# Performance work log

Measured on AMD Instinct MI355X. Metric: run time of the kernel, lower is better.

Reference implementation:

```python
import jax, jax.numpy as jnp
import numpy as np

RANK = 16
ALPHA = 16.0
IN_F = 4096
OUT_F = 11008
TOKENS = 64


def setup_inputs() -> dict:
    key = jax.random.key(0)
    k_x, k_w, k_s, k_a, k_b, k_bias = jax.random.split(key, 6)
    return {
        "x": jax.random.normal(k_x, (TOKENS, IN_F), dtype=jnp.float32),
        "weight_int4": jax.random.normal(k_w, (OUT_F, IN_F), dtype=jnp.float32),
        "weight_scale": jax.random.uniform(k_s, (OUT_F,), dtype=jnp.float32),
        "lora_A": jax.random.normal(k_a, (RANK, IN_F), dtype=jnp.float32) * 0.01,
        "lora_B": jax.random.normal(k_b, (OUT_F, RANK), dtype=jnp.float32),
        "bias": jax.random.normal(k_bias, (OUT_F,), dtype=jnp.float32),
    }


def reference(x, weight_int4, weight_scale, lora_A, lora_B, bias):
    # Dequantize: per-output-channel scale.  [out, in]
    weight = weight_int4 * weight_scale[:, None]
    # LoRA delta: B @ A scaled by alpha/rank.  [out, in]
    lora_weight = (lora_B @ lora_A) * (ALPHA / RANK)
    effective_weight = weight + lora_weight
    # F.linear: x @ W^T + b  ->  [tokens, out]
    return x @ effective_weight.T + bias
```

## Files before the change

### kernel.cpp

```cpp
#include <hip/hip_runtime.h>
#include <hip/hip_bf16.h>
#include <cstdint>

#define TOK   64
#define INF   4096
#define OUTF  11008
#define NBLK  172
#define SPLITK 4
#define KCHUNKS 128
#define KCPQ  32

using bf16x8  = __attribute__((ext_vector_type(8))) __bf16;
using floatx4 = __attribute__((ext_vector_type(4))) float;

union B8u { uint32_t u[4]; uint4 q; bf16x8 v; };

__device__ __forceinline__ uint32_t hi2(float a, float b) {
    return (__float_as_uint(a) >> 16) | (__float_as_uint(b) & 0xffff0000u);
}
__device__ __forceinline__ float losub(float x) {
    return x - __uint_as_float(__float_as_uint(x) & 0xffff0000u);
}

__global__ __launch_bounds__(256) void k_prep_x(const float* __restrict__ x,
        unsigned short* __restrict__ xh, unsigned short* __restrict__ xl) {
    int idx  = blockIdx.x * 256 + threadIdx.x;
    int j    = idx & 7;
    int lane = (idx >> 3) & 63;
    int kc   = (idx >> 9) & 127;
    int mt   = idx >> 16;
    int row  = mt * 16 + (lane & 15);
    int col  = kc * 32 + ((lane >> 4) << 3) + j;
    float v  = x[(size_t)row * INF + col];
    uint32_t u = __float_as_uint(v);
    float lo = losub(v);
    xh[idx] = (unsigned short)(u >> 16);
    xl[idx] = (unsigned short)(__float_as_uint(lo) >> 16);
}

__global__ __launch_bounds__(64) void k_lora_t(const float* __restrict__ x,
        const float* __restrict__ A, float* __restrict__ tm) {
    int t = blockIdx.x >> 4, r = blockIdx.x & 15, lane = threadIdx.x;
    const float4* xr = (const float4*)(x + (size_t)t * INF);
    const float4* ar = (const float4*)(A + (size_t)r * INF);
    float s = 0.f;
    for (int i = lane; i < INF / 4; i += 64) {
        float4 a = xr[i], b = ar[i];
        s += a.x * b.x + a.y * b.y + a.z * b.z + a.w * b.w;
    }
#pragma unroll
    for (int off = 32; off > 0; off >>= 1) s += __shfl_down(s, off);
    if (lane == 0) tm[t * 16 + r] = s;
}

template<bool ATOMIC>
__global__ __launch_bounds__(256) void k_main(const float* __restrict__ W,
        const uint4* __restrict__ xh, const uint4* __restrict__ xl,
        const float* __restrict__ scale, float* __restrict__ part,
        float* __restrict__ out) {
    int lane = threadIdx.x & 63;
    int wv   = threadIdx.x >> 6;
    int nb   = blockIdx.x % NBLK;
    int q    = blockIdx.x / NBLK;
    int orow = nb * 64 + wv * 16 + (lane & 15);
    int quad = lane >> 4;

    const float* wp = W + (size_t)orow * INF + q * (KCPQ * 32) + quad * 8;

    floatx4 acc[4] = {};

#pragma unroll 2
    for (int kc = 0; kc < KCPQ; ++kc) {
        float4 w0 = *(const float4*)(wp + (size_t)kc * 32);
        float4 w1 = *(const float4*)(wp + (size_t)kc * 32 + 4);
        B8u wh, wl;
        wh.u[0] = hi2(w0.x, w0.y);  wh.u[1] = hi2(w0.z, w0.w);
        wh.u[2] = hi2(w1.x, w1.y);  wh.u[3] = hi2(w1.z, w1.w);
        wl.u[0] = hi2(losub(w0.x), losub(w0.y));
        wl.u[1] = hi2(losub(w0.z), losub(w0.w));
        wl.u[2] = hi2(losub(w1.x), losub(w1.y));
        wl.u[3] = hi2(losub(w1.z), losub(w1.w));

        int base = (q * KCPQ + kc) * 64 + lane;
#pragma unroll
        for (int mt = 0; mt < 4; ++mt) {
            B8u ah, al;
            ah.q = xh[mt * 8192 + base];
            al.q = xl[mt * 8192 + base];
            acc[mt] = __builtin_amdgcn_mfma_f32_16x16x32_bf16(ah.v, wh.v, acc[mt], 0, 0, 0);
            acc[mt] = __builtin_amdgcn_mfma_f32_16x16x32_bf16(ah.v, wl.v, acc[mt], 0, 0, 0);
            acc[mt] = __builtin_amdgcn_mfma_f32_16x16x32_bf16(al.v, wh.v, acc[mt], 0, 0, 0);
        }
    }

#pragma unroll
    for (int mt = 0; mt < 4; ++mt) {
        int token = mt * 16 + quad * 4;
#pragma unroll
        for (int r = 0; r < 4; ++r) {
            if constexpr (ATOMIC) {
                float sc = scale[orow];
                atomicAdd(&out[(size_t)(token + r) * OUTF + orow], sc * acc[mt][r]);
            } else {
                part[((size_t)q * TOK + token + r) * OUTF + orow] = acc[mt][r];
            }
        }
    }
}

__global__ __launch_bounds__(256) void k_post(const float* __restrict__ part,
        const float* __restrict__ scale, const float* __restrict__ bias,
        const float* __restrict__ lB, const float* __restrict__ tm,
        float* __restrict__ out) {
    int o = blockIdx.x * 256 + threadIdx.x;
    int t = blockIdx.y;
    if (o >= OUTF) return;
    float s = 0.f;
#pragma unroll
    for (int qq = 0; qq < SPLITK; ++qq)
        s += part[((size_t)qq * TOK + t) * OUTF + o];
    const float4* Br = (const float4*)(lB + (size_t)o * 16);
    const float4* tr = (const float4*)(tm + (size_t)t * 16);
    float l = 0.f;
#pragma unroll
    for (int i = 0; i < 4; ++i) {
        float4 b = Br[i], tt = tr[i];
        l += b.x * tt.x + b.y * tt.y + b.z * tt.z + b.w * tt.w;
    }
    out[(size_t)t * OUTF + o] = s * scale[o] + l + bias[o];
}

__global__ __launch_bounds__(256) void k_pre(const float* __restrict__ bias,
        const float* __restrict__ lB, const float* __restrict__ tm,
        float* __restrict__ out) {
    int o = blockIdx.x * 256 + threadIdx.x;
    int t = blockIdx.y;
    if (o >= OUTF) return;
    const float4* Br = (const float4*)(lB + (size_t)o * 16);
    const float4* tr = (const float4*)(tm + (size_t)t * 16);
    float l = 0.f;
#pragma unroll
    for (int i = 0; i < 4; ++i) {
        float4 b = Br[i], tt = tr[i];
        l += b.x * tt.x + b.y * tt.y + b.z * tt.z + b.w * tt.w;
    }
    out[(size_t)t * OUTF + o] = l + bias[o];
}

extern "C" void kernel_launch(void* const* d_in, const int* in_sizes, int n_in,
                              void* d_out, int out_size, void* d_ws, size_t ws_size,
                              hipStream_t stream) {
    const float* x     = (const float*)d_in[0];
    const float* W     = (const float*)d_in[1];
    const float* scale = (const float*)d_in[2];
    const float* lA    = (const float*)d_in[3];
    const float* lB    = (const float*)d_in[4];
    const float* bias  = (const float*)d_in[5];
    float* out = (float*)d_out;

    char* ws = (char*)d_ws;
    unsigned short* xh = (unsigned short*)(ws);
    unsigned short* xl = (unsigned short*)(ws + 524288);
    float* tm   = (float*)(ws + 1048576);
    float* part = (float*)(ws + 1052672);
    const size_t need = 1052672 + (size_t)SPLITK * TOK * OUTF * 4;

    k_prep_x<<<1024, 256, 0, stream>>>(x, xh, xl);
    k_lora_t<<<1024, 64, 0, stream>>>(x, lA, tm);

    if (ws_size >= need) {
        k_main<false><<<NBLK * SPLITK, 256, 0, stream>>>(W, (const uint4*)xh,
                (const uint4*)xl, scale, part, out);
        k_post<<<dim3(43, TOK), 256, 0, stream>>>(part, scale, bias, lB, tm, out);
    } else {
        k_pre<<<dim3(43, TOK), 256, 0, stream>>>(bias, lB, tm, out);
        k_main<true><<<NBLK * SPLITK, 256, 0, stream>>>(W, (const uint4*)xh,
                (const uint4*)xl, scale, nullptr, out);
    }
}
```

Before: 328.8 us.

## Prefetch weight chunks in registers, raise split-K to 8, share x in LoRA kernel

The main GEMM kernel now keeps a four-deep register ring of fp32 weight loads, issuing the next chunk's loads before converting and multiplying the current one, so memory latency overlaps with MFMA work. Split-K rises from 4 to 8 when workspace allows, doubling the block count to 1376 to better fill the CUs for this memory-bound weight stream. The cost is twice the partial-sum traffic in the reduction kernel. The LoRA projection kernel stages each token's x row in shared memory and computes all 16 ranks per block, cutting redundant x reads.

```diff
diff --git a/kernel.cpp b/kernel.cpp
--- a/kernel.cpp
+++ b/kernel.cpp
@@ -6,9 +6,7 @@
 #define INF   4096
 #define OUTF  11008
 #define NBLK  172
-#define SPLITK 4
 #define KCHUNKS 128
-#define KCPQ  32
 
 using bf16x8  = __attribute__((ext_vector_type(8))) __bf16;
 using floatx4 = __attribute__((ext_vector_type(4))) float;
@@ -38,26 +36,35 @@
     xl[idx] = (unsigned short)(__float_as_uint(lo) >> 16);
 }
 
-__global__ __launch_bounds__(64) void k_lora_t(const float* __restrict__ x,
+__global__ __launch_bounds__(256) void k_lora_t(const float* __restrict__ x,
         const float* __restrict__ A, float* __restrict__ tm) {
-    int t = blockIdx.x >> 4, r = blockIdx.x & 15, lane = threadIdx.x;
+    __shared__ float4 xs[INF / 4];
+    int t = blockIdx.x, tid = threadIdx.x;
     const float4* xr = (const float4*)(x + (size_t)t * INF);
-    const float4* ar = (const float4*)(A + (size_t)r * INF);
-    float s = 0.f;
-    for (int i = lane; i < INF / 4; i += 64) {
-        float4 a = xr[i], b = ar[i];
-        s += a.x * b.x + a.y * b.y + a.z * b.z + a.w * b.w;
-    }
-#pragma unroll
-    for (int off = 32; off > 0; off >>= 1) s += __shfl_down(s, off);
-    if (lane == 0) tm[t * 16 + r] = s;
-}
-
-template<bool ATOMIC>
+    for (int i = tid; i < INF / 4; i += 256) xs[i] = xr[i];
+    __syncthreads();
+    int wv = tid >> 6, lane = tid & 63;
+#pragma unroll
+    for (int rr = 0; rr < 4; ++rr) {
+        int r = wv * 4 + rr;
+        const float4* ar = (const float4*)(A + (size_t)r * INF);
+        float s = 0.f;
+        for (int i = lane; i < INF / 4; i += 64) {
+            float4 a = xs[i], b = ar[i];
+            s += a.x * b.x + a.y * b.y + a.z * b.z + a.w * b.w;
+        }
+#pragma unroll
+        for (int off = 32; off > 0; off >>= 1) s += __shfl_down(s, off);
+        if (lane == 0) tm[t * 16 + r] = s;
+    }
+}
+
+template<int QCNT, bool ATOMIC>
 __global__ __launch_bounds__(256) void k_main(const float* __restrict__ W,
         const uint4* __restrict__ xh, const uint4* __restrict__ xl,
         const float* __restrict__ scale, float* __restrict__ part,
         float* __restrict__ out) {
+    constexpr int KC = KCHUNKS / QCNT;
     int lane = threadIdx.x & 63;
     int wv   = threadIdx.x >> 6;
     int nb   = blockIdx.x % NBLK;
@@ -65,31 +72,49 @@
     int orow = nb * 64 + wv * 16 + (lane & 15);
     int quad = lane >> 4;
 
-    const float* wp = W + (size_t)orow * INF + q * (KCPQ * 32) + quad * 8;
+    const float* wp = W + (size_t)orow * INF + q * (KC * 32) + quad * 8;
+    int xoff = q * KC * 64 + lane;
 
     floatx4 acc[4] = {};
 
-#pragma unroll 2
-    for (int kc = 0; kc < KCPQ; ++kc) {
-        float4 w0 = *(const float4*)(wp + (size_t)kc * 32);
-        float4 w1 = *(const float4*)(wp + (size_t)kc * 32 + 4);
-        B8u wh, wl;
-        wh.u[0] = hi2(w0.x, w0.y);  wh.u[1] = hi2(w0.z, w0.w);
-        wh.u[2] = hi2(w1.x, w1.y);  wh.u[3] = hi2(w1.z, w1.w);
-        wl.u[0] = hi2(losub(w0.x), losub(w0.y));
-        wl.u[1] = hi2(losub(w0.z), losub(w0.w));
-        wl.u[2] = hi2(losub(w1.x), losub(w1.y));
-        wl.u[3] = hi2(losub(w1.z), losub(w1.w));
-
-        int base = (q * KCPQ + kc) * 64 + lane;
-#pragma unroll
-        for (int mt = 0; mt < 4; ++mt) {
-            B8u ah, al;
-            ah.q = xh[mt * 8192 + base];
-            al.q = xl[mt * 8192 + base];
-            acc[mt] = __builtin_amdgcn_mfma_f32_16x16x32_bf16(ah.v, wh.v, acc[mt], 0, 0, 0);
-            acc[mt] = __builtin_amdgcn_mfma_f32_16x16x32_bf16(ah.v, wl.v, acc[mt], 0, 0, 0);
-            acc[mt] = __builtin_amdgcn_mfma_f32_16x16x32_bf16(al.v, wh.v, acc[mt], 0, 0, 0);
+    constexpr int D = 4;
+    float4 wA[D], wB[D];
+#pragma unroll
+    for (int d = 0; d < D; ++d) {
+        wA[d] = *(const float4*)(wp + d * 32);
+        wB[d] = *(const float4*)(wp + d * 32 + 4);
+    }
+
+#pragma unroll 1
+    for (int base = 0; base < KC; base += D) {
+#pragma unroll
+        for (int d = 0; d < D; ++d) {
+            int kc = base + d;
+            int xbase = xoff + kc * 64;
+            B8u ah[4], al[4];
+#pragma unroll
+            for (int mt = 0; mt < 4; ++mt) {
+                ah[mt].q = xh[mt * 8192 + xbase];
+                al[mt].q = xl[mt * 8192 + xbase];
+            }
+            float4 w0 = wA[d], w1 = wB[d];
+            if (base + D < KC) {
+                wA[d] = *(const float4*)(wp + (size_t)(base + D + d) * 32);
+                wB[d] = *(const float4*)(wp + (size_t)(base + D + d) * 32 + 4);
+            }
+            B8u wh, wl;
+            wh.u[0] = hi2(w0.x, w0.y);  wh.u[1] = hi2(w0.z, w0.w);
+            wh.u[2] = hi2(w1.x, w1.y);  wh.u[3] = hi2(w1.z, w1.w);
+            wl.u[0] = hi2(losub(w0.x), losub(w0.y));
+            wl.u[1] = hi2(losub(w0.z), losub(w0.w));
+            wl.u[2] = hi2(losub(w1.x), losub(w1.y));
+            wl.u[3] = hi2(losub(w1.z), losub(w1.w));
+#pragma unroll
+            for (int mt = 0; mt < 4; ++mt) {
+                acc[mt] = __builtin_amdgcn_mfma_f32_16x16x32_bf16(ah[mt].v, wh.v, acc[mt], 0, 0, 0);
+                acc[mt] = __builtin_amdgcn_mfma_f32_16x16x32_bf16(ah[mt].v, wl.v, acc[mt], 0, 0, 0);
+                acc[mt] = __builtin_amdgcn_mfma_f32_16x16x32_bf16(al[mt].v, wh.v, acc[mt], 0, 0, 0);
+            }
         }
     }
 
@@ -99,8 +124,7 @@
 #pragma unroll
         for (int r = 0; r < 4; ++r) {
             if constexpr (ATOMIC) {
-                float sc = scale[orow];
-                atomicAdd(&out[(size_t)(token + r) * OUTF + orow], sc * acc[mt][r]);
+                atomicAdd(&out[(size_t)(token + r) * OUTF + orow], scale[orow] * acc[mt][r]);
             } else {
                 part[((size_t)q * TOK + token + r) * OUTF + orow] = acc[mt][r];
             }
@@ -108,6 +132,7 @@
     }
 }
 
+template<int QCNT>
 __global__ __launch_bounds__(256) void k_post(const float* __restrict__ part,
         const float* __restrict__ scale, const float* __restrict__ bias,
         const float* __restrict__ lB, const float* __restrict__ tm,
@@ -117,7 +142,7 @@
     if (o >= OUTF) return;
     float s = 0.f;
 #pragma unroll
-    for (int qq = 0; qq < SPLITK; ++qq)
+    for (int qq = 0; qq < QCNT; ++qq)
         s += part[((size_t)qq * TOK + t) * OUTF + o];
     const float4* Br = (const float4*)(lB + (size_t)o * 16);
     const float4* tr = (const float4*)(tm + (size_t)t * 16);
@@ -163,18 +188,24 @@
     unsigned short* xl = (unsigned short*)(ws + 524288);
     float* tm   = (float*)(ws + 1048576);
     float* part = (float*)(ws + 1052672);
-    const size_t need = 1052672 + (size_t)SPLITK * TOK * OUTF * 4;
+    const size_t base_ws = 1052672;
+    const size_t need8 = base_ws + 8ull * TOK * OUTF * 4;
+    const size_t need4 = base_ws + 4ull * TOK * OUTF * 4;
 
     k_prep_x<<<1024, 256, 0, stream>>>(x, xh, xl);
-    k_lora_t<<<1024, 64, 0, stream>>>(x, lA, tm);
-
-    if (ws_size >= need) {
-        k_main<false><<<NBLK * SPLITK, 256, 0, stream>>>(W, (const uint4*)xh,
+    k_lora_t<<<TOK, 256, 0, stream>>>(x, lA, tm);
+
+    if (ws_size >= need8) {
+        k_main<8, false><<<NBLK * 8, 256, 0, stream>>>(W, (const uint4*)xh,
                 (const uint4*)xl, scale, part, out);
-        k_post<<<dim3(43, TOK), 256, 0, stream>>>(part, scale, bias, lB, tm, out);
+        k_post<8><<<dim3(43, TOK), 256, 0, stream>>>(part, scale, bias, lB, tm, out);
+    } else if (ws_size >= need4) {
+        k_main<4, false><<<NBLK * 4, 256, 0, stream>>>(W, (const uint4*)xh,
+                (const uint4*)xl, scale, part, out);
+        k_post<4><<<dim3(43, TOK), 256, 0, stream>>>(part, scale, bias, lB, tm, out);
     } else {
         k_pre<<<dim3(43, TOK), 256, 0, stream>>>(bias, lB, tm, out);
-        k_main<true><<<NBLK * SPLITK, 256, 0, stream>>>(W, (const uint4*)xh,
+        k_main<8, true><<<NBLK * 8, 256, 0, stream>>>(W, (const uint4*)xh,
                 (const uint4*)xl, scale, nullptr, out);
     }
 }
```

Result: no change. 334.7 us (+1.8%).

## Stage x tiles in LDS, widen split-K to 16, two output tiles per wave

Applied to the files above, without the earlier changes.

The main GEMM kernel now splits K 16 ways with 8 k-chunks per block. The x hi/lo bf16 tiles are loaded once into shared memory via global_load_lds, and all W loads for the chunk are issued up front. Each wave computes two 16-row output tiles, so x fragments are reused across more rows. The LoRA projection kernel is reorganised into 256-thread blocks with a fully unrolled loop. In exchange, partial-sum traffic grows (16 partial buffers of 64x11008 floats read by the post kernel), and more registers are needed to hold the prefetched W.

```diff
diff --git a/kernel.cpp b/kernel.cpp
--- a/kernel.cpp
+++ b/kernel.cpp
@@ -5,10 +5,10 @@
 #define TOK   64
 #define INF   4096
 #define OUTF  11008
-#define NBLK  172
-#define SPLITK 4
 #define KCHUNKS 128
-#define KCPQ  32
+#define QCNT  16
+#define KC    8
+#define NBLK2 86
 
 using bf16x8  = __attribute__((ext_vector_type(8))) __bf16;
 using floatx4 = __attribute__((ext_vector_type(4))) float;
@@ -20,6 +20,14 @@
 }
 __device__ __forceinline__ float losub(float x) {
     return x - __uint_as_float(__float_as_uint(x) & 0xffff0000u);
+}
+__device__ __forceinline__ void packW(float4 a, float4 b, B8u& wh, B8u& wl) {
+    wh.u[0] = hi2(a.x, a.y);  wh.u[1] = hi2(a.z, a.w);
+    wh.u[2] = hi2(b.x, b.y);  wh.u[3] = hi2(b.z, b.w);
+    wl.u[0] = hi2(losub(a.x), losub(a.y));
+    wl.u[1] = hi2(losub(a.z), losub(a.w));
+    wl.u[2] = hi2(losub(b.x), losub(b.y));
+    wl.u[3] = hi2(losub(b.z), losub(b.w));
 }
 
 __global__ __launch_bounds__(256) void k_prep_x(const float* __restrict__ x,
@@ -38,14 +46,16 @@
     xl[idx] = (unsigned short)(__float_as_uint(lo) >> 16);
 }
 
-__global__ __launch_bounds__(64) void k_lora_t(const float* __restrict__ x,
+__global__ __launch_bounds__(256) void k_lora_t(const float* __restrict__ x,
         const float* __restrict__ A, float* __restrict__ tm) {
-    int t = blockIdx.x >> 4, r = blockIdx.x & 15, lane = threadIdx.x;
+    int t = blockIdx.x, wv = threadIdx.x >> 6, lane = threadIdx.x & 63;
+    int r = blockIdx.y * 4 + wv;
     const float4* xr = (const float4*)(x + (size_t)t * INF);
     const float4* ar = (const float4*)(A + (size_t)r * INF);
     float s = 0.f;
-    for (int i = lane; i < INF / 4; i += 64) {
-        float4 a = xr[i], b = ar[i];
+#pragma unroll
+    for (int i = 0; i < INF / 4 / 64; ++i) {
+        float4 a = xr[lane + i * 64], b = ar[lane + i * 64];
         s += a.x * b.x + a.y * b.y + a.z * b.z + a.w * b.w;
     }
 #pragma unroll
@@ -54,42 +64,62 @@
 }
 
 template<bool ATOMIC>
-__global__ __launch_bounds__(256) void k_main(const float* __restrict__ W,
+__global__ __launch_bounds__(256, 2) void k_main(const float* __restrict__ W,
         const uint4* __restrict__ xh, const uint4* __restrict__ xl,
         const float* __restrict__ scale, float* __restrict__ part,
         float* __restrict__ out) {
-    int lane = threadIdx.x & 63;
-    int wv   = threadIdx.x >> 6;
-    int nb   = blockIdx.x % NBLK;
-    int q    = blockIdx.x / NBLK;
-    int orow = nb * 64 + wv * 16 + (lane & 15);
+    __shared__ uint4 xs[2][4][KC][64];
+
+    int tid  = threadIdx.x;
+    int lane = tid & 63;
+    int wv   = tid >> 6;
+    int nb   = blockIdx.x % NBLK2;
+    int q    = blockIdx.x / NBLK2;
     int quad = lane >> 4;
-
-    const float* wp = W + (size_t)orow * INF + q * (KCPQ * 32) + quad * 8;
-
-    floatx4 acc[4] = {};
-
-#pragma unroll 2
-    for (int kc = 0; kc < KCPQ; ++kc) {
-        float4 w0 = *(const float4*)(wp + (size_t)kc * 32);
-        float4 w1 = *(const float4*)(wp + (size_t)kc * 32 + 4);
-        B8u wh, wl;
-        wh.u[0] = hi2(w0.x, w0.y);  wh.u[1] = hi2(w0.z, w0.w);
-        wh.u[2] = hi2(w1.x, w1.y);  wh.u[3] = hi2(w1.z, w1.w);
-        wl.u[0] = hi2(losub(w0.x), losub(w0.y));
-        wl.u[1] = hi2(losub(w0.z), losub(w0.w));
-        wl.u[2] = hi2(losub(w1.x), losub(w1.y));
-        wl.u[3] = hi2(losub(w1.z), losub(w1.w));
-
-        int base = (q * KCPQ + kc) * 64 + lane;
+    int ch0  = nb * 128 + wv * 32 + (lane & 15);
+
+#pragma unroll
+    for (int i = 0; i < 16; ++i) {
+        int c  = wv * 16 + i;
+        int hl = c >> 5, mt = (c >> 3) & 3, kc = c & 7;
+        const uint4* g = (hl ? xl : xh)
+                       + ((size_t)mt * KCHUNKS + q * KC + kc) * 64 + lane;
+        __builtin_amdgcn_global_load_lds(
+            (const __attribute__((address_space(1))) uint32_t*)g,
+            (__attribute__((address_space(3))) uint32_t*)&xs[hl][mt][kc][0],
+            16, 0, 0);
+    }
+    __syncthreads();
+
+    const float* wp0 = W + (size_t)ch0 * INF + q * (KC * 32) + quad * 8;
+    const float* wp1 = wp0 + (size_t)16 * INF;
+    float4 w0a[KC], w0b[KC], w1a[KC], w1b[KC];
+#pragma unroll
+    for (int kc = 0; kc < KC; ++kc) {
+        w0a[kc] = *(const float4*)(wp0 + kc * 32);
+        w0b[kc] = *(const float4*)(wp0 + kc * 32 + 4);
+        w1a[kc] = *(const float4*)(wp1 + kc * 32);
+        w1b[kc] = *(const float4*)(wp1 + kc * 32 + 4);
+    }
+
+    floatx4 acc0[4] = {}, acc1[4] = {};
+
+#pragma unroll
+    for (int kc = 0; kc < KC; ++kc) {
+        B8u wh0, wl0, wh1, wl1;
+        packW(w0a[kc], w0b[kc], wh0, wl0);
+        packW(w1a[kc], w1b[kc], wh1, wl1);
 #pragma unroll
         for (int mt = 0; mt < 4; ++mt) {
             B8u ah, al;
-            ah.q = xh[mt * 8192 + base];
-            al.q = xl[mt * 8192 + base];
-            acc[mt] = __builtin_amdgcn_mfma_f32_16x16x32_bf16(ah.v, wh.v, acc[mt], 0, 0, 0);
-            acc[mt] = __builtin_amdgcn_mfma_f32_16x16x32_bf16(ah.v, wl.v, acc[mt], 0, 0, 0);
-            acc[mt] = __builtin_amdgcn_mfma_f32_16x16x32_bf16(al.v, wh.v, acc[mt], 0, 0, 0);
+            ah.q = xs[0][mt][kc][lane];
+            al.q = xs[1][mt][kc][lane];
+            acc0[mt] = __builtin_amdgcn_mfma_f32_16x16x32_bf16(ah.v, wh0.v, acc0[mt], 0, 0, 0);
+            acc0[mt] = __builtin_amdgcn_mfma_f32_16x16x32_bf16(ah.v, wl0.v, acc0[mt], 0, 0, 0);
+            acc0[mt] = __builtin_amdgcn_mfma_f32_16x16x32_bf16(al.v, wh0.v, acc0[mt], 0, 0, 0);
+            acc1[mt] = __builtin_amdgcn_mfma_f32_16x16x32_bf16(ah.v, wh1.v, acc1[mt], 0, 0, 0);
+            acc1[mt] = __builtin_amdgcn_mfma_f32_16x16x32_bf16(ah.v, wl1.v, acc1[mt], 0, 0, 0);
+            acc1[mt] = __builtin_amdgcn_mfma_f32_16x16x32_bf16(al.v, wh1.v, acc1[mt], 0, 0, 0);
         }
     }
 
@@ -99,10 +129,11 @@
 #pragma unroll
         for (int r = 0; r < 4; ++r) {
             if constexpr (ATOMIC) {
-                float sc = scale[orow];
-                atomicAdd(&out[(size_t)(token + r) * OUTF + orow], sc * acc[mt][r]);
+                atomicAdd(&out[(size_t)(token + r) * OUTF + ch0], scale[ch0] * acc0[mt][r]);
+                atomicAdd(&out[(size_t)(token + r) * OUTF + ch0 + 16], scale[ch0 + 16] * acc1[mt][r]);
             } else {
-                part[((size_t)q * TOK + token + r) * OUTF + orow] = acc[mt][r];
+                part[((size_t)q * TOK + token + r) * OUTF + ch0]      = acc0[mt][r];
+                part[((size_t)q * TOK + token + r) * OUTF + ch0 + 16] = acc1[mt][r];
             }
         }
     }
@@ -117,7 +148,7 @@
     if (o >= OUTF) return;
     float s = 0.f;
 #pragma unroll
-    for (int qq = 0; qq < SPLITK; ++qq)
+    for (int qq = 0; qq < QCNT; ++qq)
         s += part[((size_t)qq * TOK + t) * OUTF + o];
     const float4* Br = (const float4*)(lB + (size_t)o * 16);
     const float4* tr = (const float4*)(tm + (size_t)t * 16);
@@ -163,18 +194,18 @@
     unsigned short* xl = (unsigned short*)(ws + 524288);
     float* tm   = (float*)(ws + 1048576);
     float* part = (float*)(ws + 1052672);
-    const size_t need = 1052672 + (size_t)SPLITK * TOK * OUTF * 4;
+    const size_t need = 1052672 + (size_t)QCNT * TOK * OUTF * 4;
 
     k_prep_x<<<1024, 256, 0, stream>>>(x, xh, xl);
-    k_lora_t<<<1024, 64, 0, stream>>>(x, lA, tm);
+    k_lora_t<<<dim3(TOK, 4), 256, 0, stream>>>(x, lA, tm);
 
     if (ws_size >= need) {
-        k_main<false><<<NBLK * SPLITK, 256, 0, stream>>>(W, (const uint4*)xh,
+        k_main<false><<<NBLK2 * QCNT, 256, 0, stream>>>(W, (const uint4*)xh,
                 (const uint4*)xl, scale, part, out);
         k_post<<<dim3(43, TOK), 256, 0, stream>>>(part, scale, bias, lB, tm, out);
     } else {
         k_pre<<<dim3(43, TOK), 256, 0, stream>>>(bias, lB, tm, out);
-        k_main<true><<<NBLK * SPLITK, 256, 0, stream>>>(W, (const uint4*)xh,
+        k_main<true><<<NBLK2 * QCNT, 256, 0, stream>>>(W, (const uint4*)xh,
                 (const uint4*)xl, scale, nullptr, out);
     }
 }
```

Result: faster. 298.8 us (-9.1%).
